# Optimization experiments

Measured on AMD Instinct MI355X. Metric: run time of the kernel, lower is better.

The kernel has to match this reference:

```python
import jax, jax.numpy as jnp
import numpy as np


def _make_dplr(N):
    # HiPPO-NPLR -> diagonalized (p, q, lambda), matching _make_p_q_lambda
    idx = np.arange(1, N + 1)
    hippo = np.where(
        idx[:, None] > idx[None, :],
        np.sqrt(2.0 * idx[:, None] + 1.0) * np.sqrt(2.0 * idx[None, :] + 1.0),
        np.where(idx[:, None] == idx[None, :], idx[:, None] + 1.0, 0.0),
    )
    p = 0.5 * np.sqrt(2.0 * idx + 1.0)
    q = 2.0 * p
    S = -hippo + p[:, None] * q[None, :]
    lam, V = np.linalg.eig(S)
    Vc = V.conj().T
    return Vc @ p.astype(np.complex128), Vc @ q.conj().astype(np.complex128), lam


def _ri(x):
    # complex -> [..., 2] float32 (torch.view_as_real layout)
    return np.stack([x.real, x.imag], axis=-1).astype(np.float32)


def setup_inputs() -> dict:
    D_MODEL, N, L_MAX, BATCH = 512, 64, 2048, 16
    key = jax.random.key(0)
    k_u, k_B, k_Ct, k_step = jax.random.split(key, 4)
    p, q, lam = _make_dplr(N)
    std = float(np.sqrt(2.0 / (D_MODEL + N)))  # xavier_normal gain=1
    B_ri = jax.random.normal(k_B, (D_MODEL, N, 2), dtype=jnp.float32) * (std / np.sqrt(2.0))
    Ct_ri = jax.random.normal(k_Ct, (D_MODEL, N, 2), dtype=jnp.float32) * (std / np.sqrt(2.0))
    dt_min, dt_max = 1e-3, 1e-1
    log_step = (jax.random.uniform(k_step, (D_MODEL,), dtype=jnp.float32)
                * float(np.log(dt_max) - np.log(dt_min)) + float(np.log(dt_min)))
    u = jax.random.normal(k_u, (BATCH, L_MAX, D_MODEL), dtype=jnp.float32)
    return {
        'u': u,
        'p_ri': jnp.asarray(_ri(p)),
        'q_ri': jnp.asarray(_ri(q)),
        'lam_ri': jnp.asarray(_ri(lam)),
        'B_ri': B_ri,
        'Ct_ri': Ct_ri,
        'D': jnp.ones((1, 1, D_MODEL), jnp.float32),
        'log_step': log_step,
    }


def _to_c(x):
    return jax.lax.complex(x[..., 0], x[..., 1])


def reference(u, p_ri, q_ri, lam_ri, B_ri, Ct_ri, D, log_step):
    l_max = u.shape[1]
    p, q, lam = _to_c(p_ri), _to_c(q_ri), _to_c(lam_ri)
    B, Ct = _to_c(B_ri), _to_c(Ct_ri)
    # roots of unity omega_l
    omega = jnp.exp((2j * np.pi / l_max) * jnp.arange(l_max)).astype(jnp.complex64)
    step = jnp.exp(log_step)
    g = jnp.outer(2.0 / step, (1.0 - omega) / (1.0 + omega))   # [d, L] complex
    c = 2.0 / (1.0 + omega)                                    # [L]
    # fused Cauchy kernel: one reciprocal tensor shared by all four dots
    r = 1.0 / (g[:, :, None] - lam[None, None, :])             # [d, L, n]
    a0, a1, b0, b1 = Ct.conj(), q.conj(), B, p
    k00 = jnp.einsum('dn,dln->dl', a0 * b0, r)
    k01 = jnp.einsum('dn,dln->dl', a0 * b1, r)
    k10 = jnp.einsum('dn,dln->dl', a1 * b0, r)
    k11 = jnp.einsum('n,dln->dl', a1 * b1, r)
    at_roots = c * (k00 - k01 * k10 / (1.0 + k11))             # [d, L]
    out = jnp.fft.ifft(at_roots, n=l_max, axis=-1)
    # ifft reordering: [0, L-1, L-2, ..., 1]
    order = jnp.concatenate([jnp.zeros((1,), jnp.int32), jnp.arange(l_max - 1, 0, -1, dtype=jnp.int32)])
    K = out[:, order].real[None]                               # [1, d, L]
    # non-circular (linear) convolution via length-2L FFT
    ud = jnp.fft.rfft(jnp.pad(u, ((0, 0), (0, l_max), (0, 0))), axis=1)   # [B, L+1, d]
    Kd = jnp.fft.rfft(jnp.pad(K, ((0, 0), (0, 0), (0, l_max))), axis=-1)  # [1, d, L+1]
    y = jnp.fft.irfft(jnp.swapaxes(ud, -2, -1) * Kd, axis=-1)[..., :l_max]
    return jnp.swapaxes(y, -2, -1) + D * u
```

## Files before the change

### kernel.cpp

```cpp
#include <hip/hip_runtime.h>

#define LMAX   2048
#define NFFT   4096
#define DMODEL 512
#define NSTATE 64
#define NBATCH 16
#define PI_D   3.14159265358979323846
#define NT_U   512
#define NT_K   512


__device__ __forceinline__ int swz(int a) { return a ^ ((a >> 5) & 31); }

__device__ __forceinline__ float2 cmul(float2 a, float2 b) {
  return make_float2(a.x*b.x - a.y*b.y, a.x*b.y + a.y*b.x);
}

__device__ __forceinline__ float2 twget(const float2* tw, int idx) {
  float2 w = tw[idx & 2047];
  if (idx & 2048) { w.x = -w.x; w.y = -w.y; }
  return w;
}

template<int LOGN, bool INV, int NT>
__device__ float2* fft_lds(float2* src, float2* dst, const float2* tw, int tid) {
  constexpr int N = 1 << LOGN;
  constexpr int NS8 = LOGN / 3;
  constexpr int TSH = 12 - LOGN;
  const float r2 = 0.70710678118654752f;
  int s = 1;
  #pragma unroll
  for (int st = 0; st < NS8; ++st) {
    __syncthreads();
    for (int i = tid; i < (N >> 3); i += NT) {
      const int q  = i & (s - 1);
      const int ps = i - q;
      float2 x[8];
      #pragma unroll
      for (int k = 0; k < 8; ++k) x[k] = src[swz(i + k * (N >> 3))];
      float2 E0,E1,E2,E3,O0,O1,O2,O3;
      {
        float2 u0 = make_float2(x[0].x+x[4].x, x[0].y+x[4].y);
        float2 v0 = make_float2(x[0].x-x[4].x, x[0].y-x[4].y);
        float2 u1 = make_float2(x[2].x+x[6].x, x[2].y+x[6].y);
        float2 v1 = make_float2(x[2].x-x[6].x, x[2].y-x[6].y);
        E0 = make_float2(u0.x+u1.x, u0.y+u1.y);
        E2 = make_float2(u0.x-u1.x, u0.y-u1.y);
        if (!INV) { E1 = make_float2(v0.x+v1.y, v0.y-v1.x); E3 = make_float2(v0.x-v1.y, v0.y+v1.x); }
        else      { E1 = make_float2(v0.x-v1.y, v0.y+v1.x); E3 = make_float2(v0.x+v1.y, v0.y-v1.x); }
      }
      {
        float2 u0 = make_float2(x[1].x+x[5].x, x[1].y+x[5].y);
        float2 v0 = make_float2(x[1].x-x[5].x, x[1].y-x[5].y);
        float2 u1 = make_float2(x[3].x+x[7].x, x[3].y+x[7].y);
        float2 v1 = make_float2(x[3].x-x[7].x, x[3].y-x[7].y);
        O0 = make_float2(u0.x+u1.x, u0.y+u1.y);
        O2 = make_float2(u0.x-u1.x, u0.y-u1.y);
        if (!INV) { O1 = make_float2(v0.x+v1.y, v0.y-v1.x); O3 = make_float2(v0.x-v1.y, v0.y+v1.x); }
        else      { O1 = make_float2(v0.x-v1.y, v0.y+v1.x); O3 = make_float2(v0.x+v1.y, v0.y-v1.x); }
      }
      float2 o1 = (!INV) ? make_float2((O1.x+O1.y)*r2, (O1.y-O1.x)*r2)
                         : make_float2((O1.x-O1.y)*r2, (O1.y+O1.x)*r2);
      float2 o2 = (!INV) ? make_float2(O2.y, -O2.x) : make_float2(-O2.y, O2.x);
      float2 o3 = (!INV) ? make_float2((O3.y-O3.x)*r2, -(O3.x+O3.y)*r2)
                         : make_float2(-(O3.x+O3.y)*r2, (O3.x-O3.y)*r2);
      float2 y[8];
      y[0] = make_float2(E0.x+O0.x, E0.y+O0.y);
      y[4] = make_float2(E0.x-O0.x, E0.y-O0.y);
      y[1] = make_float2(E1.x+o1.x, E1.y+o1.y);
      y[5] = make_float2(E1.x-o1.x, E1.y-o1.y);
      y[2] = make_float2(E2.x+o2.x, E2.y+o2.y);
      y[6] = make_float2(E2.x-o2.x, E2.y-o2.y);
      y[3] = make_float2(E3.x+o3.x, E3.y+o3.y);
      y[7] = make_float2(E3.x-o3.x, E3.y-o3.y);
      const int idx1  = ps << TSH;
      const int obase = q + (ps << 3);
      dst[swz(obase)] = y[0];
      #pragma unroll
      for (int j = 1; j < 8; ++j) {
        float2 w = twget(tw, j * idx1);
        if (INV) w.y = -w.y;
        dst[swz(obase + j * s)] = cmul(w, y[j]);
      }
    }
    s <<= 3;
    float2* t = src; src = dst; dst = t;
  }
  if constexpr (LOGN % 3 == 2) {
    __syncthreads();
    for (int i = tid; i < (N >> 2); i += NT) {
      const int q  = i & (s - 1);
      const int ps = i - q;
      float2 x0 = src[swz(i)];
      float2 x1 = src[swz(i + (N >> 2))];
      float2 x2 = src[swz(i + (N >> 1))];
      float2 x3 = src[swz(i + 3 * (N >> 2))];
      float2 u0 = make_float2(x0.x+x2.x, x0.y+x2.y), v0 = make_float2(x0.x-x2.x, x0.y-x2.y);
      float2 u1 = make_float2(x1.x+x3.x, x1.y+x3.y), v1 = make_float2(x1.x-x3.x, x1.y-x3.y);
      float2 y0 = make_float2(u0.x+u1.x, u0.y+u1.y);
      float2 y2 = make_float2(u0.x-u1.x, u0.y-u1.y);
      float2 y1, y3;
      if (!INV) { y1 = make_float2(v0.x+v1.y, v0.y-v1.x); y3 = make_float2(v0.x-v1.y, v0.y+v1.x); }
      else      { y1 = make_float2(v0.x-v1.y, v0.y+v1.x); y3 = make_float2(v0.x+v1.y, v0.y-v1.x); }
      const int idx1  = ps << TSH;
      const int obase = q + (ps << 2);
      float2 w1 = twget(tw, idx1), w2 = twget(tw, 2*idx1), w3 = twget(tw, 3*idx1);
      if (INV) { w1.y=-w1.y; w2.y=-w2.y; w3.y=-w3.y; }
      dst[swz(obase)]         = y0;
      dst[swz(obase + s)]     = cmul(w1, y1);
      dst[swz(obase + 2*s)]   = cmul(w2, y2);
      dst[swz(obase + 3*s)]   = cmul(w3, y3);
    }
    float2* t = src; src = dst; dst = t;
  }
  __syncthreads();
  return src;
}

__global__ void twiddle_init(float2* tw) {
  int j = blockIdx.x * blockDim.x + threadIdx.x;
  if (j < NFFT/2) {
    double ang = -2.0 * PI_D * (double)j / (double)NFFT;
    double s, c;
    sincos(ang, &s, &c);
    tw[j] = make_float2((float)c, (float)s);
  }
}

__global__ __launch_bounds__(NT_K) void s4_kernel_K(
    const float* __restrict__ p_ri, const float* __restrict__ q_ri,
    const float* __restrict__ lam_ri, const float* __restrict__ B_ri,
    const float* __restrict__ Ct_ri, const float* __restrict__ log_step,
    const float2* __restrict__ twg, float2* __restrict__ Kd)
{
  __shared__ float2 A[NFFT];
  __shared__ float2 Bb[NFFT];
  __shared__ float2 tw[NFFT/2];
  const int d = blockIdx.x;
  const int tid = threadIdx.x;

  for (int j = tid; j < NFFT/2; j += NT_K) tw[j] = twg[j];

  float2* lam = Bb;
  float2* w00 = Bb + 64;
  float2* w01 = Bb + 128;
  float2* w10 = Bb + 192;
  float2* w11 = Bb + 256;
  if (tid < NSTATE) {
    const int n = tid;
    float2 la = make_float2(lam_ri[2*n], lam_ri[2*n+1]);
    float2 pp = make_float2(p_ri[2*n],  p_ri[2*n+1]);
    float2 qq = make_float2(q_ri[2*n],  q_ri[2*n+1]);
    float2 Bv = make_float2(B_ri[(d*NSTATE+n)*2],  B_ri[(d*NSTATE+n)*2+1]);
    float2 Cv = make_float2(Ct_ri[(d*NSTATE+n)*2], Ct_ri[(d*NSTATE+n)*2+1]);
    lam[n] = la;
    w00[n] = make_float2(Cv.x*Bv.x + Cv.y*Bv.y, Cv.x*Bv.y - Cv.y*Bv.x);
    w01[n] = make_float2(Cv.x*pp.x + Cv.y*pp.y, Cv.x*pp.y - Cv.y*pp.x);
    w10[n] = make_float2(qq.x*Bv.x + qq.y*Bv.y, qq.x*Bv.y - qq.y*Bv.x);
    w11[n] = make_float2(qq.x*pp.x + qq.y*pp.y, qq.x*pp.y - qq.y*pp.x);
  }
  __syncthreads();

  const float two_over_step = 2.0f / expf(log_step[d]);
  for (int l = tid; l < LMAX; l += NT_K) {
    float theta = (float)(2.0 * PI_D / (double)LMAX) * (float)l;
    float si, co;
    sincosf(theta, &si, &co);
    float dx = 1.f + co, dy = si;
    float inv = 1.0f / (dx*dx + dy*dy);
    float2 c = make_float2(2.f*dx*inv, -2.f*dy*inv);
    float nx = 1.f - co, ny = -si;
    float2 g = make_float2(two_over_step * (nx*dx + ny*dy) * inv,
                           two_over_step * (ny*dx - nx*dy) * inv);
    float2 k00 = {0,0}, k01 = {0,0}, k10 = {0,0}, k11 = {0,0};
    #pragma unroll 8
    for (int n = 0; n < NSTATE; ++n) {
      float2 la = lam[n];
      float rr = g.x - la.x, ri = g.y - la.y;
      float rinv = 1.0f / (rr*rr + ri*ri);
      float2 r = make_float2(rr*rinv, -ri*rinv);
      float2 a;
      a = w00[n]; k00.x += a.x*r.x - a.y*r.y; k00.y += a.x*r.y + a.y*r.x;
      a = w01[n]; k01.x += a.x*r.x - a.y*r.y; k01.y += a.x*r.y + a.y*r.x;
      a = w10[n]; k10.x += a.x*r.x - a.y*r.y; k10.y += a.x*r.y + a.y*r.x;
      a = w11[n]; k11.x += a.x*r.x - a.y*r.y; k11.y += a.x*r.y + a.y*r.x;
    }
    float2 s1 = make_float2(1.f + k11.x, k11.y);
    float sinv = 1.0f / (s1.x*s1.x + s1.y*s1.y);
    float2 t = cmul(k01, k10);
    float2 tdiv = make_float2((t.x*s1.x + t.y*s1.y)*sinv, (t.y*s1.x - t.x*s1.y)*sinv);
    A[swz(l)] = cmul(c, make_float2(k00.x - tdiv.x, k00.y - tdiv.y));
  }

  float2* res = fft_lds<11, false, NT_K>(A, Bb, tw, tid);
  for (int k = tid; k < NFFT; k += NT_K) {
    float kr = (k < LMAX) ? res[swz(k)].x * (1.0f / LMAX) : 0.0f;
    Bb[swz(k)] = make_float2(kr, 0.f);
  }
  float2* res2 = fft_lds<12, false, NT_K>(Bb, A, tw, tid);
  for (int f = tid; f < NFFT; f += NT_K)
    Kd[(size_t)d * NFFT + f] = res2[swz(f)];
}

__global__ __launch_bounds__(NT_U) void s4_kernel_U(
    const float* __restrict__ u, const float* __restrict__ Dp,
    const float2* __restrict__ twg, const float2* __restrict__ Kd,
    float* __restrict__ out)
{
  __shared__ float2 A[NFFT];
  __shared__ float2 Bb[NFFT];
  __shared__ float2 tw[NFFT/2];
  const int bxr = blockIdx.x;
  const int dp  = (bxr & 7) * 32 + (bxr >> 3);
  const int b   = blockIdx.y;
  const int d0  = dp * 2;
  const int tid = threadIdx.x;

  for (int j = tid; j < NFFT/2; j += NT_U) tw[j] = twg[j];

  float2 ur[4];
  const float* ubase = u + ((size_t)b * LMAX) * DMODEL + d0;
  #pragma unroll
  for (int k = 0; k < 4; ++k) {
    const int l = tid + NT_U * k;
    float2 v = *(const float2*)(ubase + (size_t)l * DMODEL);
    ur[k] = v;
    A[swz(l)] = v;
  }
  #pragma unroll
  for (int k = 4; k < 8; ++k) A[swz(tid + NT_U * k)] = make_float2(0.f, 0.f);

  float2* Z = fft_lds<12, false, NT_U>(A, Bb, tw, tid);

  const float2* K0 = Kd + (size_t)d0 * NFFT;
  const float2* K1 = K0 + NFFT;
  #pragma unroll
  for (int k = 0; k < 8; ++k) {
    const int f = tid + NT_U * k;
    float2 zf = Z[swz(f)];
    float2 zr = Z[swz((NFFT - f) & (NFFT - 1))];
    float2 u0 = make_float2(0.5f*(zf.x + zr.x), 0.5f*(zf.y - zr.y));
    float2 du = make_float2(zf.x - zr.x, zf.y + zr.y);
    float2 u1 = make_float2(0.5f*du.y, -0.5f*du.x);
    float2 y0 = cmul(u0, K0[f]);
    float2 y1 = cmul(u1, K1[f]);
    Bb[swz(f)] = make_float2(y0.x - y1.y, y0.y + y1.x);
  }

  float2* W = fft_lds<12, true, NT_U>(Bb, A, tw, tid);

  const float D0 = Dp[d0], D1 = Dp[d0 + 1];
  float* obase = out + ((size_t)b * LMAX) * DMODEL + d0;
  const float scale = 1.0f / NFFT;
  #pragma unroll
  for (int k = 0; k < 4; ++k) {
    const int l = tid + NT_U * k;
    float2 w = W[swz(l)];
    float2 o = make_float2(w.x*scale + D0*ur[k].x, w.y*scale + D1*ur[k].y);
    *(float2*)(obase + (size_t)l * DMODEL) = o;
  }
}

extern "C" void kernel_launch(void* const* d_in, const int* in_sizes, int n_in,
                              void* d_out, int out_size, void* d_ws, size_t ws_size,
                              hipStream_t stream) {
  const float* u        = (const float*)d_in[0];
  const float* p_ri     = (const float*)d_in[1];
  const float* q_ri     = (const float*)d_in[2];
  const float* lam_ri   = (const float*)d_in[3];
  const float* B_ri     = (const float*)d_in[4];
  const float* Ct_ri    = (const float*)d_in[5];
  const float* Dp       = (const float*)d_in[6];
  const float* log_step = (const float*)d_in[7];
  float* out = (float*)d_out;

  float2* tw = (float2*)d_ws;
  float2* Kd = (float2*)((char*)d_ws + (NFFT/2) * sizeof(float2));

  twiddle_init<<<8, 256, 0, stream>>>(tw);
  s4_kernel_K<<<DMODEL, NT_K, 0, stream>>>(p_ri, q_ri, lam_ri, B_ri, Ct_ri,
                                           log_step, tw, Kd);
  s4_kernel_U<<<dim3(DMODEL/2, NBATCH), NT_U, 0, stream>>>(u, Dp, tw, Kd, out);
}
```

Measured before the change: 337.8 us.

## Split kernel generation into stages and exploit real-input symmetry in the convolution

Kernel generation is split into four launches: a Cauchy kernel parallel over (d, L) using fast reciprocals, a per-channel length-L FFT, and a paired-channel length-2L FFT. The paired FFT stores the packed spectra of both channels as float4 for only half the spectrum. The convolution kernel now reads twiddles straight from global memory instead of copying them to LDS, and uses padding instead of XOR swizzling for bank conflicts. The spectrum multiply writes both conjugate-symmetric halves in place, so only half the frequencies are processed. This trades extra launches and global round trips for more parallelism in kernel generation and less LDS and work in the convolution, at some risk from uncached global twiddle reads and lower rcp precision.

New measurement: 332.3 us. No clear change (-1.6%).

```diff
diff --git a/kernel.cpp b/kernel.cpp
--- a/kernel.cpp
+++ b/kernel.cpp
@@ -6,28 +6,71 @@
 #define NSTATE 64
 #define NBATCH 16
 #define PI_D   3.14159265358979323846
-#define NT_U   512
-#define NT_K   512
-
-
-__device__ __forceinline__ int swz(int a) { return a ^ ((a >> 5) & 31); }
+#define REC_STRIDE 2050
+
+#define PAD(e) ((e) + ((e) >> 4))
+
 
 __device__ __forceinline__ float2 cmul(float2 a, float2 b) {
   return make_float2(a.x*b.x - a.y*b.y, a.x*b.y + a.y*b.x);
 }
-
-__device__ __forceinline__ float2 twget(const float2* tw, int idx) {
-  float2 w = tw[idx & 2047];
-  if (idx & 2048) { w.x = -w.x; w.y = -w.y; }
-  return w;
+__device__ __forceinline__ float rcpf(float x) { return __builtin_amdgcn_rcpf(x); }
+
+template<bool INV>
+__device__ __forceinline__ void bf8(float2 x[8]) {
+  const float r2 = 0.70710678118654752f;
+  float2 E0,E1,E2,E3,O0,O1,O2,O3;
+  {
+    float2 u0 = make_float2(x[0].x+x[4].x, x[0].y+x[4].y);
+    float2 v0 = make_float2(x[0].x-x[4].x, x[0].y-x[4].y);
+    float2 u1 = make_float2(x[2].x+x[6].x, x[2].y+x[6].y);
+    float2 v1 = make_float2(x[2].x-x[6].x, x[2].y-x[6].y);
+    E0 = make_float2(u0.x+u1.x, u0.y+u1.y);
+    E2 = make_float2(u0.x-u1.x, u0.y-u1.y);
+    if (!INV) { E1 = make_float2(v0.x+v1.y, v0.y-v1.x); E3 = make_float2(v0.x-v1.y, v0.y+v1.x); }
+    else      { E1 = make_float2(v0.x-v1.y, v0.y+v1.x); E3 = make_float2(v0.x+v1.y, v0.y-v1.x); }
+  }
+  {
+    float2 u0 = make_float2(x[1].x+x[5].x, x[1].y+x[5].y);
+    float2 v0 = make_float2(x[1].x-x[5].x, x[1].y-x[5].y);
+    float2 u1 = make_float2(x[3].x+x[7].x, x[3].y+x[7].y);
+    float2 v1 = make_float2(x[3].x-x[7].x, x[3].y-x[7].y);
+    O0 = make_float2(u0.x+u1.x, u0.y+u1.y);
+    O2 = make_float2(u0.x-u1.x, u0.y-u1.y);
+    if (!INV) { O1 = make_float2(v0.x+v1.y, v0.y-v1.x); O3 = make_float2(v0.x-v1.y, v0.y+v1.x); }
+    else      { O1 = make_float2(v0.x-v1.y, v0.y+v1.x); O3 = make_float2(v0.x+v1.y, v0.y-v1.x); }
+  }
+  float2 o1 = (!INV) ? make_float2((O1.x+O1.y)*r2, (O1.y-O1.x)*r2)
+                     : make_float2((O1.x-O1.y)*r2, (O1.y+O1.x)*r2);
+  float2 o2 = (!INV) ? make_float2(O2.y, -O2.x) : make_float2(-O2.y, O2.x);
+  float2 o3 = (!INV) ? make_float2((O3.y-O3.x)*r2, -(O3.x+O3.y)*r2)
+                     : make_float2(-(O3.x+O3.y)*r2, (O3.x-O3.y)*r2);
+  x[0] = make_float2(E0.x+O0.x, E0.y+O0.y);
+  x[4] = make_float2(E0.x-O0.x, E0.y-O0.y);
+  x[1] = make_float2(E1.x+o1.x, E1.y+o1.y);
+  x[5] = make_float2(E1.x-o1.x, E1.y-o1.y);
+  x[2] = make_float2(E2.x+o2.x, E2.y+o2.y);
+  x[6] = make_float2(E2.x-o2.x, E2.y-o2.y);
+  x[3] = make_float2(E3.x+o3.x, E3.y+o3.y);
+  x[7] = make_float2(E3.x-o3.x, E3.y-o3.y);
+}
+
+__device__ __forceinline__ void bf4(float2 x[4]) {
+  float2 u0 = make_float2(x[0].x+x[2].x, x[0].y+x[2].y);
+  float2 v0 = make_float2(x[0].x-x[2].x, x[0].y-x[2].y);
+  float2 u1 = make_float2(x[1].x+x[3].x, x[1].y+x[3].y);
+  float2 v1 = make_float2(x[1].x-x[3].x, x[1].y-x[3].y);
+  x[0] = make_float2(u0.x+u1.x, u0.y+u1.y);
+  x[2] = make_float2(u0.x-u1.x, u0.y-u1.y);
+  x[1] = make_float2(v0.x+v1.y, v0.y-v1.x);
+  x[3] = make_float2(v0.x-v1.y, v0.y+v1.x);
 }
 
 template<int LOGN, bool INV, int NT>
-__device__ float2* fft_lds(float2* src, float2* dst, const float2* tw, int tid) {
+__device__ float2* fft_lds(float2* src, float2* dst, const float2* __restrict__ tw, int tid) {
   constexpr int N = 1 << LOGN;
   constexpr int NS8 = LOGN / 3;
   constexpr int TSH = 12 - LOGN;
-  const float r2 = 0.70710678118654752f;
   int s = 1;
   #pragma unroll
   for (int st = 0; st < NS8; ++st) {
@@ -37,50 +80,16 @@
       const int ps = i - q;
       float2 x[8];
       #pragma unroll
-      for (int k = 0; k < 8; ++k) x[k] = src[swz(i + k * (N >> 3))];
-      float2 E0,E1,E2,E3,O0,O1,O2,O3;
-      {
-        float2 u0 = make_float2(x[0].x+x[4].x, x[0].y+x[4].y);
-        float2 v0 = make_float2(x[0].x-x[4].x, x[0].y-x[4].y);
-        float2 u1 = make_float2(x[2].x+x[6].x, x[2].y+x[6].y);
-        float2 v1 = make_float2(x[2].x-x[6].x, x[2].y-x[6].y);
-        E0 = make_float2(u0.x+u1.x, u0.y+u1.y);
-        E2 = make_float2(u0.x-u1.x, u0.y-u1.y);
-        if (!INV) { E1 = make_float2(v0.x+v1.y, v0.y-v1.x); E3 = make_float2(v0.x-v1.y, v0.y+v1.x); }
-        else      { E1 = make_float2(v0.x-v1.y, v0.y+v1.x); E3 = make_float2(v0.x+v1.y, v0.y-v1.x); }
-      }
-      {
-        float2 u0 = make_float2(x[1].x+x[5].x, x[1].y+x[5].y);
-        float2 v0 = make_float2(x[1].x-x[5].x, x[1].y-x[5].y);
-        float2 u1 = make_float2(x[3].x+x[7].x, x[3].y+x[7].y);
-        float2 v1 = make_float2(x[3].x-x[7].x, x[3].y-x[7].y);
-        O0 = make_float2(u0.x+u1.x, u0.y+u1.y);
-        O2 = make_float2(u0.x-u1.x, u0.y-u1.y);
-        if (!INV) { O1 = make_float2(v0.x+v1.y, v0.y-v1.x); O3 = make_float2(v0.x-v1.y, v0.y+v1.x); }
-        else      { O1 = make_float2(v0.x-v1.y, v0.y+v1.x); O3 = make_float2(v0.x+v1.y, v0.y-v1.x); }
-      }
-      float2 o1 = (!INV) ? make_float2((O1.x+O1.y)*r2, (O1.y-O1.x)*r2)
-                         : make_float2((O1.x-O1.y)*r2, (O1.y+O1.x)*r2);
-      float2 o2 = (!INV) ? make_float2(O2.y, -O2.x) : make_float2(-O2.y, O2.x);
-      float2 o3 = (!INV) ? make_float2((O3.y-O3.x)*r2, -(O3.x+O3.y)*r2)
-                         : make_float2(-(O3.x+O3.y)*r2, (O3.x-O3.y)*r2);
-      float2 y[8];
-      y[0] = make_float2(E0.x+O0.x, E0.y+O0.y);
-      y[4] = make_float2(E0.x-O0.x, E0.y-O0.y);
-      y[1] = make_float2(E1.x+o1.x, E1.y+o1.y);
-      y[5] = make_float2(E1.x-o1.x, E1.y-o1.y);
-      y[2] = make_float2(E2.x+o2.x, E2.y+o2.y);
-      y[6] = make_float2(E2.x-o2.x, E2.y-o2.y);
-      y[3] = make_float2(E3.x+o3.x, E3.y+o3.y);
-      y[7] = make_float2(E3.x-o3.x, E3.y-o3.y);
-      const int idx1  = ps << TSH;
-      const int obase = q + (ps << 3);
-      dst[swz(obase)] = y[0];
+      for (int k = 0; k < 8; ++k) x[k] = src[PAD(i + k * (N >> 3))];
+      bf8<INV>(x);
+      const int idx1 = ps << TSH;
+      const int ob   = q + (ps << 3);
+      dst[PAD(ob)] = x[0];
       #pragma unroll
       for (int j = 1; j < 8; ++j) {
-        float2 w = twget(tw, j * idx1);
+        float2 w = tw[j * idx1];
         if (INV) w.y = -w.y;
-        dst[swz(obase + j * s)] = cmul(w, y[j]);
+        dst[PAD(ob + j * s)] = cmul(w, x[j]);
       }
     }
     s <<= 3;
@@ -91,25 +100,13 @@
     for (int i = tid; i < (N >> 2); i += NT) {
       const int q  = i & (s - 1);
       const int ps = i - q;
-      float2 x0 = src[swz(i)];
-      float2 x1 = src[swz(i + (N >> 2))];
-      float2 x2 = src[swz(i + (N >> 1))];
-      float2 x3 = src[swz(i + 3 * (N >> 2))];
-      float2 u0 = make_float2(x0.x+x2.x, x0.y+x2.y), v0 = make_float2(x0.x-x2.x, x0.y-x2.y);
-      float2 u1 = make_float2(x1.x+x3.x, x1.y+x3.y), v1 = make_float2(x1.x-x3.x, x1.y-x3.y);
-      float2 y0 = make_float2(u0.x+u1.x, u0.y+u1.y);
-      float2 y2 = make_float2(u0.x-u1.x, u0.y-u1.y);
-      float2 y1, y3;
-      if (!INV) { y1 = make_float2(v0.x+v1.y, v0.y-v1.x); y3 = make_float2(v0.x-v1.y, v0.y+v1.x); }
-      else      { y1 = make_float2(v0.x-v1.y, v0.y+v1.x); y3 = make_float2(v0.x+v1.y, v0.y-v1.x); }
-      const int idx1  = ps << TSH;
-      const int obase = q + (ps << 2);
-      float2 w1 = twget(tw, idx1), w2 = twget(tw, 2*idx1), w3 = twget(tw, 3*idx1);
-      if (INV) { w1.y=-w1.y; w2.y=-w2.y; w3.y=-w3.y; }
-      dst[swz(obase)]         = y0;
-      dst[swz(obase + s)]     = cmul(w1, y1);
-      dst[swz(obase + 2*s)]   = cmul(w2, y2);
-      dst[swz(obase + 3*s)]   = cmul(w3, y3);
+      float2 x[4];
+      #pragma unroll
+      for (int k = 0; k < 4; ++k) x[k] = src[PAD(i + k * (N >> 2))];
+      bf4(x);
+      const int ob = q + (ps << 2);
+      #pragma unroll
+      for (int j = 0; j < 4; ++j) dst[PAD(ob + j * s)] = x[j];
     }
     float2* t = src; src = dst; dst = t;
   }
@@ -119,7 +116,7 @@
 
 __global__ void twiddle_init(float2* tw) {
   int j = blockIdx.x * blockDim.x + threadIdx.x;
-  if (j < NFFT/2) {
+  if (j < NFFT) {
     double ang = -2.0 * PI_D * (double)j / (double)NFFT;
     double s, c;
     sincos(ang, &s, &c);
@@ -127,25 +124,17 @@
   }
 }
 
-__global__ __launch_bounds__(NT_K) void s4_kernel_K(
+__global__ __launch_bounds__(256) void s4_cauchy(
     const float* __restrict__ p_ri, const float* __restrict__ q_ri,
     const float* __restrict__ lam_ri, const float* __restrict__ B_ri,
     const float* __restrict__ Ct_ri, const float* __restrict__ log_step,
-    const float2* __restrict__ twg, float2* __restrict__ Kd)
+    float2* __restrict__ atr)
 {
-  __shared__ float2 A[NFFT];
-  __shared__ float2 Bb[NFFT];
-  __shared__ float2 tw[NFFT/2];
+  __shared__ float2 Wg[5*64];
   const int d = blockIdx.x;
   const int tid = threadIdx.x;
-
-  for (int j = tid; j < NFFT/2; j += NT_K) tw[j] = twg[j];
-
-  float2* lam = Bb;
-  float2* w00 = Bb + 64;
-  float2* w01 = Bb + 128;
-  float2* w10 = Bb + 192;
-  float2* w11 = Bb + 256;
+  const int l = blockIdx.y * 256 + tid;
+
   if (tid < NSTATE) {
     const int n = tid;
     float2 la = make_float2(lam_ri[2*n], lam_ri[2*n+1]);
@@ -153,109 +142,150 @@
     float2 qq = make_float2(q_ri[2*n],  q_ri[2*n+1]);
     float2 Bv = make_float2(B_ri[(d*NSTATE+n)*2],  B_ri[(d*NSTATE+n)*2+1]);
     float2 Cv = make_float2(Ct_ri[(d*NSTATE+n)*2], Ct_ri[(d*NSTATE+n)*2+1]);
-    lam[n] = la;
-    w00[n] = make_float2(Cv.x*Bv.x + Cv.y*Bv.y, Cv.x*Bv.y - Cv.y*Bv.x);
-    w01[n] = make_float2(Cv.x*pp.x + Cv.y*pp.y, Cv.x*pp.y - Cv.y*pp.x);
-    w10[n] = make_float2(qq.x*Bv.x + qq.y*Bv.y, qq.x*Bv.y - qq.y*Bv.x);
-    w11[n] = make_float2(qq.x*pp.x + qq.y*pp.y, qq.x*pp.y - qq.y*pp.x);
+    Wg[n] = la;
+    Wg[64 +n] = make_float2(Cv.x*Bv.x + Cv.y*Bv.y, Cv.x*Bv.y - Cv.y*Bv.x);
+    Wg[128+n] = make_float2(Cv.x*pp.x + Cv.y*pp.y, Cv.x*pp.y - Cv.y*pp.x);
+    Wg[192+n] = make_float2(qq.x*Bv.x + qq.y*Bv.y, qq.x*Bv.y - qq.y*Bv.x);
+    Wg[256+n] = make_float2(qq.x*pp.x + qq.y*pp.y, qq.x*pp.y - qq.y*pp.x);
   }
   __syncthreads();
 
-  const float two_over_step = 2.0f / expf(log_step[d]);
-  for (int l = tid; l < LMAX; l += NT_K) {
-    float theta = (float)(2.0 * PI_D / (double)LMAX) * (float)l;
-    float si, co;
-    sincosf(theta, &si, &co);
-    float dx = 1.f + co, dy = si;
-    float inv = 1.0f / (dx*dx + dy*dy);
-    float2 c = make_float2(2.f*dx*inv, -2.f*dy*inv);
-    float nx = 1.f - co, ny = -si;
-    float2 g = make_float2(two_over_step * (nx*dx + ny*dy) * inv,
-                           two_over_step * (ny*dx - nx*dy) * inv);
-    float2 k00 = {0,0}, k01 = {0,0}, k10 = {0,0}, k11 = {0,0};
-    #pragma unroll 8
-    for (int n = 0; n < NSTATE; ++n) {
-      float2 la = lam[n];
-      float rr = g.x - la.x, ri = g.y - la.y;
-      float rinv = 1.0f / (rr*rr + ri*ri);
-      float2 r = make_float2(rr*rinv, -ri*rinv);
-      float2 a;
-      a = w00[n]; k00.x += a.x*r.x - a.y*r.y; k00.y += a.x*r.y + a.y*r.x;
-      a = w01[n]; k01.x += a.x*r.x - a.y*r.y; k01.y += a.x*r.y + a.y*r.x;
-      a = w10[n]; k10.x += a.x*r.x - a.y*r.y; k10.y += a.x*r.y + a.y*r.x;
-      a = w11[n]; k11.x += a.x*r.x - a.y*r.y; k11.y += a.x*r.y + a.y*r.x;
+  const float tos = 2.0f * rcpf(expf(log_step[d]));
+  float theta = (float)(2.0 * PI_D / (double)LMAX) * (float)l;
+  float si, co;
+  sincosf(theta, &si, &co);
+  float dx = 1.f + co, dy = si;
+  float inv = rcpf(dx*dx + dy*dy);
+  float2 cc = make_float2(2.f*dx*inv, -2.f*dy*inv);
+  float nx = 1.f - co, ny = -si;
+  float2 g = make_float2(tos*(nx*dx + ny*dy)*inv, tos*(ny*dx - nx*dy)*inv);
+
+  float2 a00 = {0,0}, a01 = {0,0}, a10 = {0,0}, a11 = {0,0};
+  for (int nc = 0; nc < NSTATE; nc += 4) {
+    float2 la[4], w0[4], w1[4], w2[4], w3[4];
+    #pragma unroll
+    for (int j=0;j<4;j++) {
+      la[j] = Wg[nc+j];      w0[j] = Wg[64+nc+j];  w1[j] = Wg[128+nc+j];
+      w2[j] = Wg[192+nc+j];  w3[j] = Wg[256+nc+j];
     }
-    float2 s1 = make_float2(1.f + k11.x, k11.y);
-    float sinv = 1.0f / (s1.x*s1.x + s1.y*s1.y);
-    float2 t = cmul(k01, k10);
-    float2 tdiv = make_float2((t.x*s1.x + t.y*s1.y)*sinv, (t.y*s1.x - t.x*s1.y)*sinv);
-    A[swz(l)] = cmul(c, make_float2(k00.x - tdiv.x, k00.y - tdiv.y));
-  }
-
-  float2* res = fft_lds<11, false, NT_K>(A, Bb, tw, tid);
-  for (int k = tid; k < NFFT; k += NT_K) {
-    float kr = (k < LMAX) ? res[swz(k)].x * (1.0f / LMAX) : 0.0f;
-    Bb[swz(k)] = make_float2(kr, 0.f);
-  }
-  float2* res2 = fft_lds<12, false, NT_K>(Bb, A, tw, tid);
-  for (int f = tid; f < NFFT; f += NT_K)
-    Kd[(size_t)d * NFFT + f] = res2[swz(f)];
-}
-
-__global__ __launch_bounds__(NT_U) void s4_kernel_U(
+    #pragma unroll
+    for (int j=0;j<4;j++) {
+      float rr = g.x - la[j].x, ri = g.y - la[j].y;
+      float rinv = rcpf(rr*rr + ri*ri);
+      float rx = rr*rinv, ry = -ri*rinv;
+      a00.x += w0[j].x*rx - w0[j].y*ry; a00.y += w0[j].x*ry + w0[j].y*rx;
+      a01.x += w1[j].x*rx - w1[j].y*ry; a01.y += w1[j].x*ry + w1[j].y*rx;
+      a10.x += w2[j].x*rx - w2[j].y*ry; a10.y += w2[j].x*ry + w2[j].y*rx;
+      a11.x += w3[j].x*rx - w3[j].y*ry; a11.y += w3[j].x*ry + w3[j].y*rx;
+    }
+  }
+  float2 s1 = make_float2(1.f + a11.x, a11.y);
+  float sinv = rcpf(s1.x*s1.x + s1.y*s1.y);
+  float2 t = cmul(a01, a10);
+  float2 tdiv = make_float2((t.x*s1.x + t.y*s1.y)*sinv, (t.y*s1.x - t.x*s1.y)*sinv);
+  atr[(size_t)d * LMAX + l] = cmul(cc, make_float2(a00.x - tdiv.x, a00.y - tdiv.y));
+}
+
+__global__ __launch_bounds__(256) void s4_fftK(
+    const float2* __restrict__ atr, const float2* __restrict__ tw,
+    float* __restrict__ Ktime)
+{
+  __shared__ float2 ZA[PAD(LMAX-1)+2], ZB[PAD(LMAX-1)+2];
+  const int d = blockIdx.x;
+  const int tid = threadIdx.x;
+  const float2* src = atr + (size_t)d * LMAX;
+  #pragma unroll
+  for (int k=0; k<8; ++k) { const int l = tid + (k<<8); ZA[PAD(l)] = src[l]; }
+  float2* Z = fft_lds<11, false, 256>(ZA, ZB, tw, tid);
+  #pragma unroll
+  for (int k=0; k<8; ++k) {
+    const int kk = tid + (k<<8);
+    Ktime[(size_t)d * LMAX + kk] = Z[PAD(kk)].x * (1.0f / LMAX);
+  }
+}
+
+__global__ __launch_bounds__(512) void s4_pairB(
+    const float* __restrict__ Ktime, const float2* __restrict__ tw,
+    float4* __restrict__ Kd)
+{
+  __shared__ float2 ZA[PAD(NFFT-1)+2], ZB[PAD(NFFT-1)+2];
+  const int dp = blockIdx.x;
+  const int tid = threadIdx.x;
+  const float* K0p = Ktime + (size_t)(2*dp) * LMAX;
+  const float* K1p = K0p + LMAX;
+  #pragma unroll
+  for (int il=0; il<4; ++il) {
+    const int kk = tid + (il<<9);
+    ZA[PAD(kk)] = make_float2(K0p[kk], K1p[kk]);
+    ZA[PAD(LMAX + kk)] = make_float2(0.f, 0.f);
+  }
+  float2* Z = fft_lds<12, false, 512>(ZA, ZB, tw, tid);
+  float4* rec = Kd + (size_t)dp * REC_STRIDE;
+  #pragma unroll
+  for (int it=0; it<5; ++it) {
+    int t = tid + (it<<9);
+    if (it == 4) { if (tid != 0) break; t = 2048; }
+    float2 zf = Z[PAD(t)];
+    float2 zr = Z[PAD((NFFT - t) & (NFFT-1))];
+    float k0x = 0.5f*(zf.x + zr.x), k0y = 0.5f*(zf.y - zr.y);
+    float dx = zf.x - zr.x, dy = zf.y + zr.y;
+    rec[t] = make_float4(k0x, k0y, 0.5f*dy, -0.5f*dx);
+  }
+}
+
+__global__ __launch_bounds__(512) void s4_conv(
     const float* __restrict__ u, const float* __restrict__ Dp,
-    const float2* __restrict__ twg, const float2* __restrict__ Kd,
+    const float2* __restrict__ tw, const float4* __restrict__ Kd,
     float* __restrict__ out)
 {
-  __shared__ float2 A[NFFT];
-  __shared__ float2 Bb[NFFT];
-  __shared__ float2 tw[NFFT/2];
+  __shared__ float2 ZA[PAD(NFFT-1)+2], ZB[PAD(NFFT-1)+2];
   const int bxr = blockIdx.x;
   const int dp  = (bxr & 7) * 32 + (bxr >> 3);
   const int b   = blockIdx.y;
   const int d0  = dp * 2;
   const int tid = threadIdx.x;
 
-  for (int j = tid; j < NFFT/2; j += NT_U) tw[j] = twg[j];
-
   float2 ur[4];
   const float* ubase = u + ((size_t)b * LMAX) * DMODEL + d0;
   #pragma unroll
-  for (int k = 0; k < 4; ++k) {
-    const int l = tid + NT_U * k;
+  for (int k=0; k<4; ++k) {
+    const int l = tid + (k<<9);
     float2 v = *(const float2*)(ubase + (size_t)l * DMODEL);
     ur[k] = v;
-    A[swz(l)] = v;
-  }
-  #pragma unroll
-  for (int k = 4; k < 8; ++k) A[swz(tid + NT_U * k)] = make_float2(0.f, 0.f);
-
-  float2* Z = fft_lds<12, false, NT_U>(A, Bb, tw, tid);
-
-  const float2* K0 = Kd + (size_t)d0 * NFFT;
-  const float2* K1 = K0 + NFFT;
-  #pragma unroll
-  for (int k = 0; k < 8; ++k) {
-    const int f = tid + NT_U * k;
-    float2 zf = Z[swz(f)];
-    float2 zr = Z[swz((NFFT - f) & (NFFT - 1))];
+    ZA[PAD(l)] = v;
+    ZA[PAD(LMAX + l)] = make_float2(0.f, 0.f);
+  }
+
+  float2* Z = fft_lds<12, false, 512>(ZA, ZB, tw, tid);
+
+  const float4* rec = Kd + (size_t)dp * REC_STRIDE;
+  #pragma unroll
+  for (int it=0; it<5; ++it) {
+    int t = tid + (it<<9);
+    if (it == 4) { if (tid != 0) break; t = 2048; }
+    const int j1 = PAD(t);
+    const int j2 = PAD((NFFT - t) & (NFFT-1));
+    float2 zf = Z[j1], zr = Z[j2];
+    float4 r4 = rec[t];
+    float2 K0 = make_float2(r4.x, r4.y), K1 = make_float2(r4.z, r4.w);
     float2 u0 = make_float2(0.5f*(zf.x + zr.x), 0.5f*(zf.y - zr.y));
-    float2 du = make_float2(zf.x - zr.x, zf.y + zr.y);
-    float2 u1 = make_float2(0.5f*du.y, -0.5f*du.x);
-    float2 y0 = cmul(u0, K0[f]);
-    float2 y1 = cmul(u1, K1[f]);
-    Bb[swz(f)] = make_float2(y0.x - y1.y, y0.y + y1.x);
-  }
-
-  float2* W = fft_lds<12, true, NT_U>(Bb, A, tw, tid);
+    float du_x = zf.x - zr.x, du_y = zf.y + zr.y;
+    float2 u1 = make_float2(0.5f*du_y, -0.5f*du_x);
+    float2 P = cmul(u0, K0);
+    float2 Q = cmul(u1, K1);
+    Z[j1] = make_float2(P.x - Q.y, P.y + Q.x);
+    Z[j2] = make_float2(P.x + Q.y, Q.x - P.y);
+  }
+
+  float2* W = fft_lds<12, true, 512>(Z, (Z == ZA) ? ZB : ZA, tw, tid);
 
   const float D0 = Dp[d0], D1 = Dp[d0 + 1];
   float* obase = out + ((size_t)b * LMAX) * DMODEL + d0;
   const float scale = 1.0f / NFFT;
   #pragma unroll
-  for (int k = 0; k < 4; ++k) {
-    const int l = tid + NT_U * k;
-    float2 w = W[swz(l)];
+  for (int k=0; k<4; ++k) {
+    const int l = tid + (k<<9);
+    float2 w = W[PAD(l)];
     float2 o = make_float2(w.x*scale + D0*ur[k].x, w.y*scale + D1*ur[k].y);
     *(float2*)(obase + (size_t)l * DMODEL) = o;
   }
@@ -274,11 +304,17 @@
   const float* log_step = (const float*)d_in[7];
   float* out = (float*)d_out;
 
-  float2* tw = (float2*)d_ws;
-  float2* Kd = (float2*)((char*)d_ws + (NFFT/2) * sizeof(float2));
-
-  twiddle_init<<<8, 256, 0, stream>>>(tw);
-  s4_kernel_K<<<DMODEL, NT_K, 0, stream>>>(p_ri, q_ri, lam_ri, B_ri, Ct_ri,
-                                           log_step, tw, Kd);
-  s4_kernel_U<<<dim3(DMODEL/2, NBATCH), NT_U, 0, stream>>>(u, Dp, tw, Kd, out);
-}
+  char* wsb = (char*)d_ws;
+  float2* tw    = (float2*)wsb;
+  float4* Kd    = (float4*)(wsb + NFFT * sizeof(float2));
+  float2* atr   = (float2*)Kd;
+  float*  Ktime = (float*)(wsb + NFFT * sizeof(float2)
+                               + (size_t)256 * REC_STRIDE * sizeof(float4));
+
+  twiddle_init<<<16, 256, 0, stream>>>(tw);
+  s4_cauchy<<<dim3(DMODEL, 8), 256, 0, stream>>>(p_ri, q_ri, lam_ri, B_ri, Ct_ri,
+                                                 log_step, atr);
+  s4_fftK<<<DMODEL, 256, 0, stream>>>(atr, tw, Ktime);
+  s4_pairB<<<DMODEL/2, 512, 0, stream>>>(Ktime, tw, Kd);
+  s4_conv<<<dim3(DMODEL/2, NBATCH), 512, 0, stream>>>(u, Dp, tw, Kd, out);
+}
```
